# Optimization experiments

Hardware: AMD Instinct MI355X
Metric: run time of the kernel (lower is better)

## Reference

```python
import jax, jax.numpy as jnp
import numpy as np

IN_DIM = 256
OUT_DIM = 256
GRID_SIZE = 8
K = 3  # spline_order
LOW, UP = -1.0, 1.0
BATCH = 512


def _control_grid():
    # equally spaced control points, extended by K on each side (paper sec 2.4)
    spacing = (UP - LOW) / GRID_SIZE
    g = jnp.arange(-K, GRID_SIZE + K + 1, dtype=jnp.float32) * spacing + LOW
    # buffer shape (out_dim, in_dim, G + 2K + 1)
    return jnp.broadcast_to(g[None, None, :], (OUT_DIM, IN_DIM, g.shape[0]))


def _bspline_bases(x, grid):
    # x: (B, in_dim); grid: (out, in, T). Cox-de Boor recursion.
    xx = x[:, None, :, None]          # (B, 1, in, 1)
    g = grid[None]                    # (1, out, in, T)
    # order-0 (piecewise-constant) bases
    b = ((xx >= g[..., :-1]) & (xx < g[..., 1:])).astype(x.dtype)
    for j in range(1, K + 1):
        b = (xx - g[..., :-(j + 1)]) / (g[..., j:-1] - g[..., :-(j + 1)]) * b[..., :-1] \
          + (g[..., j + 1:] - xx) / (g[..., j + 1:] - g[..., 1:-j]) * b[..., 1:]
    return b  # (B, out, in, G + K)


def setup_inputs() -> dict:
    key = jax.random.key(0)
    k1, k2, k3 = jax.random.split(key, 3)
    x = jax.random.normal(k1, (BATCH, IN_DIM), dtype=jnp.float32)
    # xavier_normal_ on (out, in, G+K): fan_in = in*(G+K) -> std = sqrt(2/(fan_in+fan_out))
    fan_out = IN_DIM * (GRID_SIZE + K)  # torch convention: dim0 = fan_out, rest = fan_in
    fan_in = OUT_DIM * (GRID_SIZE + K)
    std = float(np.sqrt(2.0 / (fan_in + fan_out)))
    coef = jax.random.normal(k2, (OUT_DIM, IN_DIM, GRID_SIZE + K), dtype=jnp.float32) * std
    residual_weight = jax.random.normal(k3, (OUT_DIM, IN_DIM), dtype=jnp.float32) * 0.1
    univariate_weight = jnp.ones((OUT_DIM, IN_DIM), dtype=jnp.float32)
    return {"x": x, "coef": coef, "residual_weight": residual_weight,
            "univariate_weight": univariate_weight}


def reference(x, coef, residual_weight, univariate_weight):
    grid = _control_grid()
    bases = _bspline_bases(x, grid)                      # (B, out, in, G+K)
    spline = jnp.einsum('boig,oig->boi', bases, coef)    # sum over grid dim
    phi = residual_weight[None, :, :] * jax.nn.silu(x)[:, None, :] \
        + univariate_weight[None, :, :] * spline          # (B, out, in)
    return jnp.sum(phi, axis=-1)                          # (B, out)
```

## Files before the change

kernel.cpp:

```cpp
#include <hip/hip_runtime.h>
#include <hip/hip_bf16.h>

typedef unsigned short ushort_t;
typedef unsigned int uint_t;
typedef __attribute__((ext_vector_type(8))) short short8;
typedef __attribute__((ext_vector_type(4))) float f32x4;

#define IN_DIM 256
#define OUT_DIM 256
#define NSPL 11
#define KSLOT 12
#define CHUNK_I 32
#define KC (CHUNK_I * KSLOT)
#define LSTRIDE (KC + 8)
#define NCHUNK 8
#define RAWF 356

__device__ __forceinline__ uint_t pk2(float lo, float hi) {
  __hip_bfloat162 h = __float22bfloat162_rn(make_float2(lo, hi));
  union { __hip_bfloat162 h2; uint_t u; } c; c.h2 = h;
  return c.u;
}

__device__ __forceinline__ void packA_scatter(ushort_t* cb, ushort_t* dump, float xf) {
  const float t = (xf + 1.75f) * 4.0f;
  const float fJ = floorf(t);
  const int J = (int)fJ;
  const float u = t - fJ;
  const float u2 = u * u, u3 = u2 * u, um = 1.0f - u;
  const float n0 = um * um * um * (1.0f / 6.0f);
  const float n1 = 0.5f * u3 - u2 + (4.0f / 6.0f);
  const float n2 = -0.5f * u3 + 0.5f * u2 + 0.5f * u + (1.0f / 6.0f);
  const float n3 = u3 * (1.0f / 6.0f);
  const float silu = xf / (1.0f + __expf(-xf));

#pragma unroll
  for (int z = 0; z < 12; ++z) cb[z] = 0;

  const uint_t p01 = pk2(n0, n1);
  const uint_t p23 = pk2(n2, n3);
  const uint_t psl = pk2(silu, silu);

  const int base = J - 3;
  ushort_t* w0 = ((unsigned)(base + 0) <= 10u) ? (cb + base + 0) : (dump + 0);
  ushort_t* w1 = ((unsigned)(base + 1) <= 10u) ? (cb + base + 1) : (dump + 1);
  ushort_t* w2 = ((unsigned)(base + 2) <= 10u) ? (cb + base + 2) : (dump + 2);
  ushort_t* w3 = ((unsigned)(base + 3) <= 10u) ? (cb + base + 3) : (dump + 3);
  *w0 = (ushort_t)p01;
  *w1 = (ushort_t)(p01 >> 16);
  *w2 = (ushort_t)p23;
  *w3 = (ushort_t)(p23 >> 16);
  cb[11] = (ushort_t)psl;
}

__device__ __forceinline__ void packW_f32(const float* c, float us, float r, uint_t o6[6]) {
  o6[0] = pk2(us * c[0], us * c[1]);
  o6[1] = pk2(us * c[2], us * c[3]);
  o6[2] = pk2(us * c[4], us * c[5]);
  o6[3] = pk2(us * c[6], us * c[7]);
  o6[4] = pk2(us * c[8], us * c[9]);
  o6[5] = pk2(us * c[10], r);
}

__device__ __forceinline__ void writeT(ushort_t* dst, const uint_t* p) {
  uint_t* d = (uint_t*)dst;
#pragma unroll
  for (int j = 0; j < 6; ++j) d[j] = p[j];
}

__global__ __launch_bounds__(256, 2) void fused(const float* __restrict__ x,
                                                const float* __restrict__ coef,
                                                const float* __restrict__ rw,
                                                const float* __restrict__ uw,
                                                float* __restrict__ out) {
  __shared__ __attribute__((aligned(16))) ushort_t As[2][16 * LSTRIDE];
  __shared__ __attribute__((aligned(16))) ushort_t Ws[2][16 * LSTRIDE];
  __shared__ __attribute__((aligned(16))) float rawc[16][RAWF];

  const int tid = threadIdx.x;
  const int lane = tid & 63;
  const int w = tid >> 6;
  const int B = blockIdx.x;
  const int mt = B >> 4;
  const int nt = ((B & 7) << 1) | ((B >> 3) & 1);
  const int b0 = mt * 16, o0 = nt * 16;
  const int mn = lane & 15;
  const int klane = (lane >> 4) * 8;

  const int row = tid >> 4;
  const int i0 = tid & 15;

  float2 cfA[11], cfB[11];
  float xaA0, xaA1, usA0, usA1, rrA0, rrA1;
  float xaB0, xaB1, usB0, usB1, rrB0, rrB1;

#define LOADC(S, C)                                                           \
  {                                                                           \
    const int ib = (C) * CHUNK_I;                                             \
    xa##S##0 = x[(b0 + row) * IN_DIM + ib + i0];                              \
    xa##S##1 = x[(b0 + row) * IN_DIM + ib + i0 + 16];                         \
    const int orow = o0 + row;                                                \
    us##S##0 = uw[orow * IN_DIM + ib + i0];                                   \
    us##S##1 = uw[orow * IN_DIM + ib + i0 + 16];                              \
    rr##S##0 = rw[orow * IN_DIM + ib + i0];                                   \
    rr##S##1 = rw[orow * IN_DIM + ib + i0 + 16];                              \
    const float2* csrc = (const float2*)(coef + ((size_t)orow * IN_DIM + ib) * NSPL); \
    _Pragma("unroll")                                                         \
    for (int j = 0; j < 11; ++j) cf##S[j] = csrc[i0 + j * 16];   \
  }

#define CVTPACK(S, BUF)                                                       \
  {                                                                           \
    float2* rrow = (float2*)&rawc[row][0];                                    \
    _Pragma("unroll")                                                         \
    for (int j = 0; j < 11; ++j) rrow[i0 + j * 16] = cf##S[j];                \
    ushort_t* arow = &As[BUF][row * LSTRIDE];                                 \
    packA_scatter(arow + i0 * KSLOT, arow + KC, xa##S##0);                    \
    packA_scatter(arow + (i0 + 16) * KSLOT, arow + KC, xa##S##1);             \
    uint_t p6[6];                                                             \
    packW_f32(&rawc[row][NSPL * i0], us##S##0, rr##S##0, p6);                 \
    writeT(&Ws[BUF][row * LSTRIDE + i0 * KSLOT], p6);                         \
    packW_f32(&rawc[row][NSPL * (i0 + 16)], us##S##1, rr##S##1, p6);          \
    writeT(&Ws[BUF][row * LSTRIDE + (i0 + 16) * KSLOT], p6);                  \
  }

#define MFMA3(BUF)                                                            \
  {                                                                           \
    _Pragma("unroll")                                                         \
    for (int q = 0; q < 3; ++q) {                                             \
      const int k = w * 96 + q * 32 + klane;                                  \
      short8 af  = *(const short8*)&As[BUF][mn * LSTRIDE + k];                \
      short8 bfr = *(const short8*)&Ws[BUF][mn * LSTRIDE + k];                \
      acc = __builtin_amdgcn_mfma_f32_16x16x32_bf16(af, bfr, acc, 0, 0, 0);   \
    }                                                                         \
  }

  f32x4 acc = {0.f, 0.f, 0.f, 0.f};

  LOADC(A, 0)
  CVTPACK(A, 0)
  LOADC(B, 1)
  __syncthreads();

#pragma unroll
  for (int cc = 0; cc < 4; ++cc) {
    MFMA3(0)
    if (cc < 3) { LOADC(A, 2 * cc + 2) }
    CVTPACK(B, 1)
    __syncthreads();

    MFMA3(1)
    if (cc < 3) {
      LOADC(B, 2 * cc + 3)
      CVTPACK(A, 0)
    }
    __syncthreads();
  }

  f32x4* red = (f32x4*)&rawc[0][0];
  if (w > 0) red[(w - 1) * 64 + lane] = acc;
  __syncthreads();

  if (w == 0) {
    const f32x4 q0 = red[lane];
    const f32x4 q1 = red[64 + lane];
    const f32x4 q2 = red[128 + lane];
#pragma unroll
    for (int q = 0; q < 4; ++q) acc[q] += q0[q] + q1[q] + q2[q];

    const int col = o0 + mn;
    const int rbase = b0 + (lane >> 4) * 4;
#pragma unroll
    for (int r = 0; r < 4; ++r) {
      out[(size_t)(rbase + r) * OUT_DIM + col] = acc[r];
    }
  }
}

extern "C" void kernel_launch(void* const* d_in, const int* in_sizes, int n_in,
                              void* d_out, int out_size, void* d_ws, size_t ws_size,
                              hipStream_t stream) {
  const float* x    = (const float*)d_in[0];
  const float* coef = (const float*)d_in[1];
  const float* rw   = (const float*)d_in[2];
  const float* uw   = (const float*)d_in[3];
  float* out = (float*)d_out;

  fused<<<512, 256, 0, stream>>>(x, coef, rw, uw, out);
}
```

Baseline: 18.67 us.

## Pack spline weights directly from registers, drop LDS staging of raw coefficients

Removes the rawc shared-memory staging buffer for coefficients. Each thread now multiplies its coalesced float2 coef loads by the matching univariate weight, fetched per element through a precomputed divide-by-11 index, and scatters bf16 results straight into the W tile. Shared memory drops enough to allow raising launch bounds to 3 blocks per CU. The cost is more uw gathers, more registers, and 2-byte scattered LDS stores that may bank-conflict.

```diff
diff --git a/kernel.cpp b/kernel.cpp
--- a/kernel.cpp
+++ b/kernel.cpp
@@ -14,7 +14,6 @@
 #define KC (CHUNK_I * KSLOT)
 #define LSTRIDE (KC + 8)
 #define NCHUNK 8
-#define RAWF 356
 
 __device__ __forceinline__ uint_t pk2(float lo, float hi) {
   __hip_bfloat162 h = __float22bfloat162_rn(make_float2(lo, hi));
@@ -53,29 +52,14 @@
   cb[11] = (ushort_t)psl;
 }
 
-__device__ __forceinline__ void packW_f32(const float* c, float us, float r, uint_t o6[6]) {
-  o6[0] = pk2(us * c[0], us * c[1]);
-  o6[1] = pk2(us * c[2], us * c[3]);
-  o6[2] = pk2(us * c[4], us * c[5]);
-  o6[3] = pk2(us * c[6], us * c[7]);
-  o6[4] = pk2(us * c[8], us * c[9]);
-  o6[5] = pk2(us * c[10], r);
-}
-
-__device__ __forceinline__ void writeT(ushort_t* dst, const uint_t* p) {
-  uint_t* d = (uint_t*)dst;
-#pragma unroll
-  for (int j = 0; j < 6; ++j) d[j] = p[j];
-}
-
-__global__ __launch_bounds__(256, 2) void fused(const float* __restrict__ x,
+__global__ __launch_bounds__(256, 3) void fused(const float* __restrict__ x,
                                                 const float* __restrict__ coef,
                                                 const float* __restrict__ rw,
                                                 const float* __restrict__ uw,
                                                 float* __restrict__ out) {
   __shared__ __attribute__((aligned(16))) ushort_t As[2][16 * LSTRIDE];
   __shared__ __attribute__((aligned(16))) ushort_t Ws[2][16 * LSTRIDE];
-  __shared__ __attribute__((aligned(16))) float rawc[16][RAWF];
+  __shared__ __attribute__((aligned(16))) f32x4 red[3][64];
 
   const int tid = threadIdx.x;
   const int lane = tid & 63;
@@ -90,38 +74,58 @@
   const int row = tid >> 4;
   const int i0 = tid & 15;
 
+  const float* x_p  = x  + (size_t)(b0 + row) * IN_DIM;
+  const int orow = o0 + row;
+  const float* uw_p = uw + (size_t)orow * IN_DIM;
+  const float* rw_p = rw + (size_t)orow * IN_DIM;
+  const float* cf_p = coef + (size_t)orow * IN_DIM * NSPL;
+
+  int q0[11], q1[11];
+#pragma unroll
+  for (int j = 0; j < 11; ++j) {
+    const int e0 = 2 * i0 + 32 * j;
+    q0[j] = (e0 * 5958) >> 16;
+    q1[j] = ((e0 + 1) * 5958) >> 16;
+  }
+
   float2 cfA[11], cfB[11];
-  float xaA0, xaA1, usA0, usA1, rrA0, rrA1;
-  float xaB0, xaB1, usB0, usB1, rrB0, rrB1;
+  float usA0[11], usA1[11], usB0[11], usB1[11];
+  float xaA0, xaA1, rrA0, rrA1;
+  float xaB0, xaB1, rrB0, rrB1;
 
 #define LOADC(S, C)                                                           \
   {                                                                           \
     const int ib = (C) * CHUNK_I;                                             \
-    xa##S##0 = x[(b0 + row) * IN_DIM + ib + i0];                              \
-    xa##S##1 = x[(b0 + row) * IN_DIM + ib + i0 + 16];                         \
-    const int orow = o0 + row;                                                \
-    us##S##0 = uw[orow * IN_DIM + ib + i0];                                   \
-    us##S##1 = uw[orow * IN_DIM + ib + i0 + 16];                              \
-    rr##S##0 = rw[orow * IN_DIM + ib + i0];                                   \
-    rr##S##1 = rw[orow * IN_DIM + ib + i0 + 16];                              \
-    const float2* csrc = (const float2*)(coef + ((size_t)orow * IN_DIM + ib) * NSPL); \
+    xa##S##0 = x_p[ib + i0];                                                  \
+    xa##S##1 = x_p[ib + i0 + 16];                                             \
+    rr##S##0 = rw_p[ib + i0];                                                 \
+    rr##S##1 = rw_p[ib + i0 + 16];                                            \
+    const float2* csrc = (const float2*)(cf_p + (size_t)ib * NSPL);           \
     _Pragma("unroll")                                                         \
-    for (int j = 0; j < 11; ++j) cf##S[j] = csrc[i0 + j * 16];   \
+    for (int j = 0; j < 11; ++j) cf##S[j] = csrc[i0 + j * 16];                \
+    _Pragma("unroll")                                                         \
+    for (int j = 0; j < 11; ++j) {                                            \
+      us##S##0[j] = uw_p[ib + q0[j]];                                         \
+      us##S##1[j] = uw_p[ib + q1[j]];                                         \
+    }                                                                         \
   }
 
 #define CVTPACK(S, BUF)                                                       \
   {                                                                           \
-    float2* rrow = (float2*)&rawc[row][0];                                    \
-    _Pragma("unroll")                                                         \
-    for (int j = 0; j < 11; ++j) rrow[i0 + j * 16] = cf##S[j];                \
     ushort_t* arow = &As[BUF][row * LSTRIDE];                                 \
     packA_scatter(arow + i0 * KSLOT, arow + KC, xa##S##0);                    \
     packA_scatter(arow + (i0 + 16) * KSLOT, arow + KC, xa##S##1);             \
-    uint_t p6[6];                                                             \
-    packW_f32(&rawc[row][NSPL * i0], us##S##0, rr##S##0, p6);                 \
-    writeT(&Ws[BUF][row * LSTRIDE + i0 * KSLOT], p6);                         \
-    packW_f32(&rawc[row][NSPL * (i0 + 16)], us##S##1, rr##S##1, p6);          \
-    writeT(&Ws[BUF][row * LSTRIDE + (i0 + 16) * KSLOT], p6);                  \
+    ushort_t* wrow = &Ws[BUF][row * LSTRIDE];                                 \
+    _Pragma("unroll")                                                         \
+    for (int j = 0; j < 11; ++j) {                                            \
+      const int e0 = 2 * i0 + 32 * j;                                         \
+      const uint_t pv = pk2(us##S##0[j] * cf##S[j].x,                         \
+                            us##S##1[j] * cf##S[j].y);                        \
+      wrow[e0 + q0[j]]     = (ushort_t)pv;                                    \
+      wrow[e0 + 1 + q1[j]] = (ushort_t)(pv >> 16);                            \
+    }                                                                         \
+    wrow[i0 * KSLOT + 11]        = (ushort_t)pk2(rr##S##0, rr##S##0);         \
+    wrow[(i0 + 16) * KSLOT + 11] = (ushort_t)pk2(rr##S##1, rr##S##1);         \
   }
 
 #define MFMA3(BUF)                                                            \
@@ -157,16 +161,15 @@
     __syncthreads();
   }
 
-  f32x4* red = (f32x4*)&rawc[0][0];
-  if (w > 0) red[(w - 1) * 64 + lane] = acc;
+  if (w > 0) red[w - 1][lane] = acc;
   __syncthreads();
 
   if (w == 0) {
-    const f32x4 q0 = red[lane];
-    const f32x4 q1 = red[64 + lane];
-    const f32x4 q2 = red[128 + lane];
+    const f32x4 t0 = red[0][lane];
+    const f32x4 t1 = red[1][lane];
+    const f32x4 t2 = red[2][lane];
 #pragma unroll
-    for (int q = 0; q < 4; ++q) acc[q] += q0[q] + q1[q] + q2[q];
+    for (int q = 0; q < 4; ++q) acc[q] += t0[q] + t1[q] + t2[q];
 
     const int col = o0 + mn;
     const int rbase = b0 + (lane >> 4) * 4;
```

Result: slower. 32.19 us (+72.4%).
